# Kernel tuning notes

Measured on AMD Instinct MI355X. Metric: run time of the kernel, lower is better.

The kernel has to match this reference:

```python
import jax, jax.numpy as jnp
import numpy as np

N = 50000      # nodes
E = 800000     # message-passing edges
EF = 1000000   # decoder (full) edges
IN = 128       # in_channels
H = 64         # hidden_channels
OUT = 1        # out_channels
T = 128        # num_timesteps
RESCALE = 4000.0  # SinusoidalPosEmb rescale_steps


def sinusoidal_pos_emb(t, dim, num_steps):
    # t: [N] int -> [N, dim]
    x = t.astype(jnp.float32) * (RESCALE / num_steps)
    half = dim // 2
    freqs = jnp.exp(jnp.arange(half, dtype=jnp.float32) * (-jnp.log(10000.0) / (half - 1)))
    ang = x[:, None] * freqs[None, :]            # [N, half]
    return jnp.concatenate([jnp.sin(ang), jnp.cos(ang)], axis=-1)


def gcn_conv(h, W, b, row, col, norm, n):
    # standard GCNConv: linear -> gather src -> scale by sym norm -> scatter-add to dst -> +bias
    x = h @ W                                     # [N, H]
    msg = x[row] * norm[:, None]                  # [E+N, H]
    out = jax.ops.segment_sum(msg, col, num_segments=n)
    return out + b


def setup_inputs() -> dict:
    key = jax.random.key(0)
    ks = jax.random.split(key, 12)
    rn = lambda k, shape, s=0.02: jax.random.normal(k, shape, jnp.float32) * s
    return {
        "x": jax.random.normal(ks[0], (N, IN), jnp.float32),
        "edge_index": jax.random.randint(ks[1], (2, E), 0, N, jnp.int32),
        "full_edge_index": jax.random.randint(ks[2], (2, EF), 0, N, jnp.int32),
        "time_steps": jax.random.randint(ks[3], (N,), 0, T, jnp.int32),
        "W_in": rn(ks[4], (IN, H)), "b_in": jnp.zeros((H,), jnp.float32),
        "W_t1": rn(ks[5], (H, 4 * H)), "b_t1": jnp.zeros((4 * H,), jnp.float32),
        "W_t2": rn(ks[6], (4 * H, H)), "b_t2": jnp.zeros((H,), jnp.float32),
        "W_c0": rn(ks[7], (H, H)), "b_c0": jnp.zeros((H,), jnp.float32),
        "W_c1": rn(ks[8], (H, H)), "b_c1": jnp.zeros((H,), jnp.float32),
        "W_d1": rn(ks[9], (2 * H, H)), "b_d1": jnp.zeros((H,), jnp.float32),
        "W_d2": rn(ks[10], (H, OUT)), "b_d2": jnp.zeros((OUT,), jnp.float32),
    }


def reference(x, edge_index, full_edge_index, time_steps,
              W_in, b_in, W_t1, b_t1, W_t2, b_t2,
              W_c0, b_c0, W_c1, b_c1, W_d1, b_d1, W_d2, b_d2):
    n = x.shape[0]
    # --- embedder (dropout is identity in eval mode) ---
    h = x @ W_in + b_in                                        # [N, H]
    pe = sinusoidal_pos_emb(time_steps, H, T)                  # [N, H]
    t_emb = jax.nn.silu(pe @ W_t1 + b_t1) @ W_t2 + b_t2        # [N, H]
    h_embed = h + t_emb

    # --- GCN encoder: add self-loops once, symmetric normalization ---
    loops = jnp.arange(n, dtype=edge_index.dtype)
    row = jnp.concatenate([edge_index[0], loops])              # [E+N]
    col = jnp.concatenate([edge_index[1], loops])
    deg = jax.ops.segment_sum(jnp.ones_like(col, jnp.float32), col, num_segments=n)
    dinv = jnp.where(deg > 0, jax.lax.rsqrt(deg), 0.0)
    norm = dinv[row] * dinv[col]                               # [E+N]

    h = gcn_conv(h_embed, W_c0, b_c0, row, col, norm, n)
    h = jax.nn.relu(h)                                         # act between layers; norm=None -> identity
    h_enc = gcn_conv(h, W_c1, b_c1, row, col, norm, n)

    # --- edge decoder: gather src/dst, concat, 2-layer SiLU MLP ---
    src, dst = full_edge_index[0], full_edge_index[1]
    feat = jnp.concatenate([h_enc[src], h_enc[dst]], axis=-1)  # [EF, 2H]
    edge_logits = jax.nn.silu(feat @ W_d1 + b_d1) @ W_d2 + b_d2  # [EF, OUT]
    return edge_logits, h_embed, h_enc
```

## Files before the change

### kernel.cpp

```cpp
#include <hip/hip_runtime.h>
#include <hip/hip_bf16.h>
#include <math.h>

#define N_NODES 50000
#define E_MSG   800000
#define E_FULL  1000000
#define IN_C    128
#define H_C     64
#define T_STEPS 128

#define OFF_Win   0
#define OFF_bin   8192
#define OFF_Wt1   8256
#define OFF_bt1   24640
#define OFF_Wt2   24896
#define OFF_bt2   41280
#define OFF_Wc0   41344
#define OFF_bc0   45440
#define OFF_Wc1   45504
#define OFF_bc1   49600
#define OFF_Wd1   49664
#define OFF_bd1   57856
#define OFF_Wd2   57920
#define OFF_bd2   57984
#define W_TOTAL   57985
#define OFF_BSUM  58016
#define OFF_BCUR  58272
#define OFF_FWD1  58624
#define OFF_FWIN  60672
#define OFF_FWC0  64768
#define OFF_TEMB  66816
#define OFF_DINV  75008
#define OFF_FWC1  125008
#define OFF_PTR   175008
#define OFF_ELIST 225010
#define OFF_TMP2  1025012
#define OFF_ZBF   2625012
#define OFF_ZBF2  4225012
#define OFF_HENC8 5825012

#define SCAN_NB   ((N_NODES + 255) / 256)
#define BF_CH     ((E_MSG + SCAN_NB - 1) / SCAN_NB)
#define BC_NB     392
#define BC_CH     ((E_MSG + BC_NB - 1) / BC_NB)

typedef __attribute__((ext_vector_type(8))) short bf16x8;
typedef __attribute__((ext_vector_type(4))) float f32x4;

static __device__ __forceinline__ float bf2f(unsigned short u) {
    return __uint_as_float(((unsigned)u) << 16);
}
static __device__ __forceinline__ unsigned short f2bf(float f) {
    unsigned u = __float_as_uint(f);
    unsigned r = (u + 0x7fffu + ((u >> 16) & 1u)) >> 16;
    return (unsigned short)r;
}
static __device__ __forceinline__ unsigned char f2fp8(float f) {
    unsigned u = __float_as_uint(f);
    unsigned s = (u >> 24) & 0x80;
    float a = fminf(__uint_as_float(u & 0x7FFFFFFF), 448.0f);
    if (a < 0.015625f) {
        int qi = (int)rintf(a * 512.0f);
        return (unsigned char)(s | qi);
    }
    unsigned ua = __float_as_uint(a);
    int e = (int)((ua >> 23) & 0xFF) - 127;
    unsigned man = (ua & 0x7FFFFF) | 0x800000;
    unsigned r = man >> 20;
    unsigned rem = man & 0xFFFFF;
    if (rem > 0x80000u || (rem == 0x80000u && (r & 1))) r++;
    if (r == 16) { r = 8; e++; }
    if (e > 8) return (unsigned char)(s | 0x7E);
    return (unsigned char)(s | ((unsigned)(e + 7) << 3) | (r & 7));
}
static __device__ __forceinline__ bool detect_f32(const unsigned short* w, int* scnt) {
    if (threadIdx.x == 0) *scnt = 0;
    __syncthreads();
    int big = 0;
    for (int i = threadIdx.x; i < 2048; i += blockDim.x)
        if (fabsf(bf2f(w[2 * i])) > 0.5f) big++;
    atomicAdd(scnt, big);
    __syncthreads();
    return *scnt > 64;
}
static __device__ __forceinline__ float ldw(const void* p, int idx, bool f32) {
    return f32 ? ((const float*)p)[idx] : bf2f(((const unsigned short*)p)[idx]);
}

__global__ void __launch_bounds__(256) k_bfill(const int* __restrict__ row,
                                               const int* __restrict__ col,
                                               const int* __restrict__ btot,
                                               int* __restrict__ bcur,
                                               uint2* __restrict__ tmp) {
    __shared__ int pref[256];
    __shared__ int hist[SCAN_NB];
    __shared__ int basew[SCAN_NB];
    int b = blockIdx.x, t = threadIdx.x;

    int tv = (t < SCAN_NB) ? btot[t] : 0;
    pref[t] = tv;
    __syncthreads();
    for (int off = 1; off < 256; off <<= 1) {
        int u = (t >= off) ? pref[t - off] : 0;
        __syncthreads();
        pref[t] += u;
        __syncthreads();
    }
    int excl_t = pref[t] - tv;

    int lo = b * BF_CH;
    int hi = lo + BF_CH; if (hi > E_MSG) hi = E_MSG;
    for (int i = t; i < SCAN_NB; i += 256) hist[i] = 0;
    __syncthreads();
    for (int e = lo + t; e < hi; e += 256)
        atomicAdd(&hist[col[e] >> 8], 1);
    __syncthreads();
    if (t < SCAN_NB) {
        int c = hist[t];
        basew[t] = (c > 0) ? excl_t + atomicAdd(&bcur[t], c) : 0;
    }
    __syncthreads();
    for (int i = t; i < SCAN_NB; i += 256) hist[i] = 0;
    __syncthreads();
    for (int e = lo + t; e < hi; e += 256) {
        int src = row[e], c = col[e];
        int bk = c >> 8;
        int off = atomicAdd(&hist[bk], 1);
        tmp[basew[bk] + off] = uint2{(unsigned)src, (unsigned)c};
    }
}

__global__ void __launch_bounds__(256) k_csort2(const uint2* __restrict__ tmp,
                                                const int* __restrict__ btot,
                                                int* __restrict__ ptr,
                                                float* __restrict__ dinv,
                                                int* __restrict__ elist) {
    __shared__ int deg[256];
    __shared__ int pfx[256];
    int b = blockIdx.x, t = threadIdx.x;

    int tv = (t < SCAN_NB) ? btot[t] : 0;
    pfx[t] = tv;
    __syncthreads();
    for (int off = 1; off < 256; off <<= 1) {
        int u = (t >= off) ? pfx[t - off] : 0;
        __syncthreads();
        pfx[t] += u;
        __syncthreads();
    }
    __shared__ int se[2];
    if (t == b) { se[0] = pfx[t] - tv; se[1] = pfx[t]; }
    __syncthreads();
    int start = se[0], end = se[1];

    deg[t] = 0;
    __syncthreads();
    for (int e = start + t; e < end; e += 256)
        atomicAdd(&deg[tmp[e].y & 255], 1);
    __syncthreads();

    int v = deg[t];
    pfx[t] = v;
    __syncthreads();
    for (int off = 1; off < 256; off <<= 1) {
        int u = (t >= off) ? pfx[t - off] : 0;
        __syncthreads();
        pfx[t] += u;
        __syncthreads();
    }
    int excl = pfx[t] - v;
    int n = (b << 8) + t;
    if (n < N_NODES) {
        ptr[n] = start + excl;
        dinv[n] = rsqrtf((float)v + 1.0f);
    }
    if (b == 0 && t == 0) ptr[N_NODES] = E_MSG;
    __syncthreads();
    deg[t] = excl;
    __syncthreads();
    for (int e = start + t; e < end; e += 256) {
        uint2 p = tmp[e];
        int pos = atomicAdd(&deg[p.y & 255], 1);
        elist[start + pos] = (int)p.x;
    }
}

#define WP_BC_NB   392
#define WP_CVT_NB  227
#define WP_PREP_NB 96
#define WP_TEMB_NB 128
#define WP_TOTAL_NB (WP_BC_NB + WP_CVT_NB + WP_PREP_NB + WP_TEMB_NB)

struct CvtArgs { const void* src[14]; };

__global__ void __launch_bounds__(256) k_wprep(CvtArgs a,
                                               const int* __restrict__ ecol,
                                               int* __restrict__ bsum,
                                               float* ws) {
    __shared__ int scnt;
    int bid = blockIdx.x;
    int tid = threadIdx.x;

    if (bid < WP_BC_NB) {
        __shared__ int hist[SCAN_NB];
        for (int i = tid; i < SCAN_NB; i += 256) hist[i] = 0;
        __syncthreads();
        int lo = bid * BC_CH;
        int hi = lo + BC_CH; if (hi > E_MSG) hi = E_MSG;
        for (int e = lo + tid; e < hi; e += 256)
            atomicAdd(&hist[ecol[e] >> 8], 1);
        __syncthreads();
        for (int i = tid; i < SCAN_NB; i += 256) {
            int c = hist[i];
            if (c > 0) atomicAdd(&bsum[i], c);
        }
        return;
    }
    bid -= WP_BC_NB;

    bool f32 = detect_f32((const unsigned short*)a.src[0], &scnt);

    if (bid < WP_CVT_NB) {
        int t = bid * 256 + tid;
        if (t >= W_TOTAL) return;
        const int starts[14] = {OFF_Win, OFF_bin, OFF_Wt1, OFF_bt1, OFF_Wt2, OFF_bt2,
                                OFF_Wc0, OFF_bc0, OFF_Wc1, OFF_bc1, OFF_Wd1, OFF_bd1,
                                OFF_Wd2, OFF_bd2};
        int seg = 0;
#pragma unroll
        for (int i = 1; i < 14; i++)
            if (t >= starts[i]) seg = i;
        ws[t] = ldw(a.src[seg], t - starts[seg], f32);
    } else if (bid < WP_CVT_NB + WP_PREP_NB) {
        int idx = (bid - WP_CVT_NB) * 256 + tid;
        int local, j, lane, ct, c, t, m, q;
        if (idx < 8192) {
            local = idx;
            j = local & 7; lane = (local >> 3) & 63; ct = local >> 9;
            c = ct >> 2; t = ct & 3; m = lane & 15; q = lane >> 4;
            ((unsigned char*)(ws + OFF_FWD1))[local] =
                f2fp8(16.0f * ldw(a.src[10], (32 * c + 8 * q + j) * 64 + 16 * t + m, f32));
        } else if (idx < 16384) {
            local = idx - 8192;
            j = local & 7; lane = (local >> 3) & 63; ct = local >> 9;
            c = ct >> 2; t = ct & 3; m = lane & 15; q = lane >> 4;
            ((unsigned short*)(ws + OFF_FWIN))[local] =
                f2bf(ldw(a.src[0], (32 * c + 8 * q + j) * 64 + 16 * t + m, f32));
        } else if (idx < 20480) {
            local = idx - 16384;
            j = local & 7; lane = (local >> 3) & 63; ct = local >> 9;
            c = ct >> 2; t = ct & 3; m = lane & 15; q = lane >> 4;
            ((unsigned short*)(ws + OFF_FWC0))[local] =
                f2bf(ldw(a.src[6], (32 * c + 8 * q + j) * 64 + 16 * t + m, f32));
        } else {
            local = idx - 20480;
            j = local & 7; lane = (local >> 3) & 63; ct = local >> 9;
            c = ct >> 2; t = ct & 3; m = lane & 15; q = lane >> 4;
            ((unsigned short*)(ws + OFF_FWC1))[local] =
                f2bf(ldw(a.src[8], (32 * c + 8 * q + j) * 64 + 16 * t + m, f32));
        }
    } else {
        __shared__ float pe[64];
        __shared__ float us4[4][256];
        __shared__ float us[256];
        __shared__ float pcs[4][64];
        int j = tid & 63;
        int kg = tid >> 6;
        int t = bid - WP_CVT_NB - WP_PREP_NB;

        if (tid < 64) {
            float xt = (float)t * (4000.0f / 128.0f);
            float sc = -logf(10000.0f) / 31.0f;
            float fr = __expf((float)(tid & 31) * sc);
            float ang = xt * fr;
            pe[tid] = (tid < 32) ? sinf(ang) : cosf(ang);
        }
        __syncthreads();

        float pu[4] = {0.f, 0.f, 0.f, 0.f};
#pragma unroll
        for (int kk = 0; kk < 16; kk++) {
            int k = 16 * kg + kk;
            float p = pe[k];
#pragma unroll
            for (int q = 0; q < 4; q++)
                pu[q] = fmaf(p, ldw(a.src[2], k * 256 + q * 64 + j, f32), pu[q]);
        }
#pragma unroll
        for (int q = 0; q < 4; q++) us4[kg][q * 64 + j] = pu[q];
        __syncthreads();

        {
            float uu = ldw(a.src[3], tid, f32) +
                       us4[0][tid] + us4[1][tid] + us4[2][tid] + us4[3][tid];
            us[tid] = uu * __builtin_amdgcn_rcpf(1.0f + __expf(-uu));
        }
        __syncthreads();

        float pc = 0.f;
#pragma unroll
        for (int kk = 0; kk < 64; kk++) {
            int k = 64 * kg + kk;
            pc = fmaf(us[k], ldw(a.src[4], k * 64 + j, f32), pc);
        }
        pcs[kg][j] = pc;
        __syncthreads();
        if (tid < 64) {
            float acc = ldw(a.src[5], j, f32) +
                        pcs[0][j] + pcs[1][j] + pcs[2][j] + pcs[3][j];
            (ws + OFF_TEMB)[t * 64 + j] = acc;
        }
    }
}

__global__ void __launch_bounds__(256) k_embed(const void* __restrict__ xraw,
                                               const unsigned short* __restrict__ wdet,
                                               const int* __restrict__ tsteps,
                                               float* __restrict__ ws,
                                               float* __restrict__ out_hembed,
                                               unsigned short* __restrict__ zbf) {
    __shared__ int scnt;
    __shared__ unsigned short tl[4][16 * 64];
    bool f32 = detect_f32(wdet, &scnt);

    int lane = threadIdx.x & 63;
    int wv = threadIdx.x >> 6;
    int m = lane & 15, quad = lane >> 4;
    int wid = blockIdx.x * 4 + wv;
    if (wid > N_NODES / 16 - 1) wid = N_NODES / 16 - 1;
    int n0 = wid * 16;

    const unsigned short* fwin = (const unsigned short*)(ws + OFF_FWIN);
    const unsigned short* fwc0 = (const unsigned short*)(ws + OFF_FWC0);

    bf16x8 bI[4][4];
#pragma unroll
    for (int c = 0; c < 4; c++)
#pragma unroll
        for (int t = 0; t < 4; t++)
            bI[c][t] = *reinterpret_cast<const bf16x8*>(fwin + (c * 4 + t) * 512 + lane * 8);

    f32x4 acc[4] = {f32x4{0,0,0,0}, f32x4{0,0,0,0}, f32x4{0,0,0,0}, f32x4{0,0,0,0}};
#pragma unroll
    for (int c = 0; c < 4; c++) {
        bf16x8 a;
        if (f32) {
            const float* xp = (const float*)xraw + (size_t)(n0 + m) * 128 + 32 * c + 8 * quad;
            float4 v0 = *reinterpret_cast<const float4*>(xp);
            float4 v1 = *reinterpret_cast<const float4*>(xp + 4);
            a[0] = (short)f2bf(v0.x); a[1] = (short)f2bf(v0.y);
            a[2] = (short)f2bf(v0.z); a[3] = (short)f2bf(v0.w);
            a[4] = (short)f2bf(v1.x); a[5] = (short)f2bf(v1.y);
            a[6] = (short)f2bf(v1.z); a[7] = (short)f2bf(v1.w);
        } else {
            a = *reinterpret_cast<const bf16x8*>(
                (const unsigned short*)xraw + (size_t)(n0 + m) * 128 + 32 * c + 8 * quad);
        }
#pragma unroll
        for (int t = 0; t < 4; t++)
            acc[t] = __builtin_amdgcn_mfma_f32_16x16x32_bf16(a, bI[c][t], acc[t], 0, 0, 0);
    }

    int tn[4];
#pragma unroll
    for (int r = 0; r < 4; r++) tn[r] = tsteps[n0 + 4 * quad + r];
    const float* temb = ws + OFF_TEMB;
#pragma unroll
    for (int t = 0; t < 4; t++) {
        int ch = 16 * t + m;
        float bj = ws[OFF_bin + ch];
#pragma unroll
        for (int r = 0; r < 4; r++) {
            int node = n0 + 4 * quad + r;
            float v = acc[t][r] + bj + temb[tn[r] * 64 + ch];
            out_hembed[(size_t)node * 64 + ch] = v;
            tl[wv][(4 * quad + r) * 64 + ch] = f2bf(v);
        }
    }
    __syncthreads();

    bf16x8 bC[2][4];
#pragma unroll
    for (int c = 0; c < 2; c++)
#pragma unroll
        for (int t = 0; t < 4; t++)
            bC[c][t] = *reinterpret_cast<const bf16x8*>(fwc0 + (c * 4 + t) * 512 + lane * 8);

    f32x4 az[4] = {f32x4{0,0,0,0}, f32x4{0,0,0,0}, f32x4{0,0,0,0}, f32x4{0,0,0,0}};
#pragma unroll
    for (int c = 0; c < 2; c++) {
        bf16x8 a2 = *reinterpret_cast<const bf16x8*>(&tl[wv][m * 64 + 32 * c + 8 * quad]);
#pragma unroll
        for (int t = 0; t < 4; t++)
            az[t] = __builtin_amdgcn_mfma_f32_16x16x32_bf16(a2, bC[c][t], az[t], 0, 0, 0);
    }
    const float* dinv = ws + OFF_DINV;
    float dv[4];
#pragma unroll
    for (int r = 0; r < 4; r++) dv[r] = dinv[n0 + 4 * quad + r];
#pragma unroll
    for (int t = 0; t < 4; t++) {
        int ch = 16 * t + m;
#pragma unroll
        for (int r = 0; r < 4; r++)
            zbf[(size_t)(n0 + 4 * quad + r) * 64 + ch] = f2bf(az[t][r] * dv[r]);
    }
}

__global__ void __launch_bounds__(256) k_gather0(const unsigned short* __restrict__ zbf,
                                                 const int* __restrict__ ptr,
                                                 const int* __restrict__ elist,
                                                 const float* __restrict__ ws,
                                                 unsigned short* __restrict__ zout) {
    __shared__ unsigned short tile[16 * 64];
    const float* dinv = ws + OFF_DINV;
    const float* bias = ws + OFF_bc0;
    const unsigned short* fwc1 = (const unsigned short*)(ws + OFF_FWC1);

    int lane = threadIdx.x & 63;
    int wv = threadIdx.x >> 6;
    int g = lane >> 4;
    int cl = lane & 15;
    int n0 = blockIdx.x * 16;

    float4 b4 = *reinterpret_cast<const float4*>(bias + 4 * cl);

#pragma unroll
    for (int snode = 0; snode < 4; snode++) {
        int li = wv * 4 + snode;
        int n = n0 + li;
        int base = ptr[n], end = ptr[n + 1];

        float ws0 = (g == 0) ? 1.0f : 0.0f;
        ushort4 sv = *reinterpret_cast<const ushort4*>(zbf + (size_t)n * 64 + cl * 4);
        float s0 = ws0 * bf2f(sv.x), s1 = ws0 * bf2f(sv.y);
        float s2 = ws0 * bf2f(sv.z), s3 = ws0 * bf2f(sv.w);

        for (int k = base; k < end; k += 8) {
            int e0 = k + g, e1 = k + 4 + g;
            int r0 = elist[min(e0, end - 1)];
            int r1 = elist[min(e1, end - 1)];
            ushort4 v0 = *reinterpret_cast<const ushort4*>(zbf + (size_t)r0 * 64 + cl * 4);
            ushort4 v1 = *reinterpret_cast<const ushort4*>(zbf + (size_t)r1 * 64 + cl * 4);
            float w0 = (e0 < end) ? 1.0f : 0.0f;
            float w1 = (e1 < end) ? 1.0f : 0.0f;
            s0 = fmaf(w0, bf2f(v0.x), s0); s1 = fmaf(w0, bf2f(v0.y), s1);
            s2 = fmaf(w0, bf2f(v0.z), s2); s3 = fmaf(w0, bf2f(v0.w), s3);
            s0 = fmaf(w1, bf2f(v1.x), s0); s1 = fmaf(w1, bf2f(v1.y), s1);
            s2 = fmaf(w1, bf2f(v1.z), s2); s3 = fmaf(w1, bf2f(v1.w), s3);
        }
        s0 += __shfl_xor(s0, 16, 64); s0 += __shfl_xor(s0, 32, 64);
        s1 += __shfl_xor(s1, 16, 64); s1 += __shfl_xor(s1, 32, 64);
        s2 += __shfl_xor(s2, 16, 64); s2 += __shfl_xor(s2, 32, 64);
        s3 += __shfl_xor(s3, 16, 64); s3 += __shfl_xor(s3, 32, 64);

        if (g == 0) {
            float dv = dinv[n];
            float h0 = fmaxf(fmaf(dv, s0, b4.x), 0.0f);
            float h1 = fmaxf(fmaf(dv, s1, b4.y), 0.0f);
            float h2 = fmaxf(fmaf(dv, s2, b4.z), 0.0f);
            float h3 = fmaxf(fmaf(dv, s3, b4.w), 0.0f);
            ushort4 hv;
            hv.x = f2bf(h0); hv.y = f2bf(h1); hv.z = f2bf(h2); hv.w = f2bf(h3);
            int bo = li * 128 + ((cl * 8) ^ ((li & 7) << 4));
            *reinterpret_cast<ushort4*>((char*)tile + bo) = hv;
        }
    }
    __syncthreads();

    int m = lane & 15, q = lane >> 4;
    bf16x8 bB0 = *reinterpret_cast<const bf16x8*>(fwc1 + (0 * 4 + wv) * 512 + lane * 8);
    bf16x8 bB1 = *reinterpret_cast<const bf16x8*>(fwc1 + (1 * 4 + wv) * 512 + lane * 8);

    f32x4 az = f32x4{0, 0, 0, 0};
    {
        int bo0 = m * 128 + ((0 * 64 + q * 16) ^ ((m & 7) << 4));
        bf16x8 a0 = *reinterpret_cast<const bf16x8*>((const char*)tile + bo0);
        az = __builtin_amdgcn_mfma_f32_16x16x32_bf16(a0, bB0, az, 0, 0, 0);
        int bo1 = m * 128 + ((1 * 64 + q * 16) ^ ((m & 7) << 4));
        bf16x8 a1 = *reinterpret_cast<const bf16x8*>((const char*)tile + bo1);
        az = __builtin_amdgcn_mfma_f32_16x16x32_bf16(a1, bB1, az, 0, 0, 0);
    }
    float dv4[4];
#pragma unroll
    for (int r = 0; r < 4; r++) dv4[r] = dinv[n0 + 4 * q + r];
#pragma unroll
    for (int r = 0; r < 4; r++) {
        int node = n0 + 4 * q + r;
        zout[(size_t)node * 64 + 16 * wv + m] = f2bf(az[r] * dv4[r]);
    }
}

__global__ void __launch_bounds__(256) k_gather1(const unsigned short* __restrict__ zbf,
                                                 const int* __restrict__ ptr,
                                                 const int* __restrict__ elist,
                                                 const float* __restrict__ dinv,
                                                 const float* __restrict__ bias,
                                                 unsigned char* __restrict__ henc8,
                                                 float* __restrict__ ofp) {
    int lane = threadIdx.x & 63;
    int n = blockIdx.x * 4 + (threadIdx.x >> 6);
    int g = lane >> 4;
    int cl = lane & 15;
    int base = ptr[n], end = ptr[n + 1];

    float4 b4 = *reinterpret_cast<const float4*>(bias + 4 * cl);

    float ws0 = (g == 0) ? 1.0f : 0.0f;
    ushort4 sv = *reinterpret_cast<const ushort4*>(zbf + (size_t)n * 64 + cl * 4);
    float s0 = ws0 * bf2f(sv.x), s1 = ws0 * bf2f(sv.y);
    float s2 = ws0 * bf2f(sv.z), s3 = ws0 * bf2f(sv.w);

    for (int k = base; k < end; k += 8) {
        int e0 = k + g, e1 = k + 4 + g;
        int r0 = elist[min(e0, end - 1)];
        int r1 = elist[min(e1, end - 1)];
        ushort4 v0 = *reinterpret_cast<const ushort4*>(zbf + (size_t)r0 * 64 + cl * 4);
        ushort4 v1 = *reinterpret_cast<const ushort4*>(zbf + (size_t)r1 * 64 + cl * 4);
        float w0 = (e0 < end) ? 1.0f : 0.0f;
        float w1 = (e1 < end) ? 1.0f : 0.0f;
        s0 = fmaf(w0, bf2f(v0.x), s0); s1 = fmaf(w0, bf2f(v0.y), s1);
        s2 = fmaf(w0, bf2f(v0.z), s2); s3 = fmaf(w0, bf2f(v0.w), s3);
        s0 = fmaf(w1, bf2f(v1.x), s0); s1 = fmaf(w1, bf2f(v1.y), s1);
        s2 = fmaf(w1, bf2f(v1.z), s2); s3 = fmaf(w1, bf2f(v1.w), s3);
    }
    s0 += __shfl_xor(s0, 16, 64); s0 += __shfl_xor(s0, 32, 64);
    s1 += __shfl_xor(s1, 16, 64); s1 += __shfl_xor(s1, 32, 64);
    s2 += __shfl_xor(s2, 16, 64); s2 += __shfl_xor(s2, 32, 64);
    s3 += __shfl_xor(s3, 16, 64); s3 += __shfl_xor(s3, 32, 64);

    float dv = dinv[n];
    float o0 = fmaf(dv, s0, b4.x);
    float o1 = fmaf(dv, s1, b4.y);
    float o2 = fmaf(dv, s2, b4.z);
    float o3 = fmaf(dv, s3, b4.w);

    if (g == 0) {
        float4 ov; ov.x = o0; ov.y = o1; ov.z = o2; ov.w = o3;
        *reinterpret_cast<float4*>(ofp + (size_t)n * 64 + cl * 4) = ov;
    }
    int jc = lane >> 2;
    float a0 = __shfl(o0, jc, 64);
    float a1 = __shfl(o1, jc, 64);
    float a2 = __shfl(o2, jc, 64);
    float a3 = __shfl(o3, jc, 64);
    int sel = lane & 3;
    float mv = (sel == 0) ? a0 : (sel == 1) ? a1 : (sel == 2) ? a2 : a3;
    henc8[(size_t)n * 64 + lane] = f2fp8(16.0f * mv);
}

#define DEC_TPW 4
#define DEC_TILES (E_FULL / 16)

__global__ void __launch_bounds__(256) k_dec(const int* __restrict__ src,
                                             const int* __restrict__ dst,
                                             const unsigned char* __restrict__ h8,
                                             const float* __restrict__ ws,
                                             float* __restrict__ out) {
    __shared__ long s_bfr[16 * 64];
    __shared__ float s_w2[64];
    __shared__ float s_b1[64];

    int tid = threadIdx.x;
    float b2 = ws[OFF_bd2];
    {
        const long* fw8 = (const long*)(ws + OFF_FWD1);
        for (int idx = tid; idx < 1024; idx += 256)
            s_bfr[idx] = fw8[idx];
        if (tid < 64) {
            s_w2[tid] = ws[OFF_Wd2 + tid];
            s_b1[tid] = ws[OFF_bd1 + tid];
        }
    }
    __syncthreads();

    int lane = tid & 63;
    int wv = tid >> 6;
    int m = lane & 15;
    int quad = lane >> 4;

    int tile0 = (blockIdx.x * 4 + wv) * DEC_TPW;

    int sg[DEC_TPW], dg[DEC_TPW];
#pragma unroll
    for (int i = 0; i < DEC_TPW; i++) {
        int tc = min(tile0 + i, DEC_TILES - 1);
        sg[i] = src[tc * 16 + m];
        dg[i] = dst[tc * 16 + m];
    }

#pragma unroll
    for (int i = 0; i < DEC_TPW; i++) {
        int tile = tile0 + i;
        long A[4];
#pragma unroll
        for (int c = 0; c < 4; c++) {
            int row = (c < 2) ? sg[i] : dg[i];
            A[c] = *reinterpret_cast<const long*>(
                h8 + (size_t)row * 64 + (c & 1) * 32 + 8 * quad);
        }
        f32x4 acc[4] = {f32x4{0,0,0,0}, f32x4{0,0,0,0}, f32x4{0,0,0,0}, f32x4{0,0,0,0}};
#pragma unroll
        for (int c = 0; c < 4; c++)
#pragma unroll
            for (int mt = 0; mt < 4; mt++) {
                long bk = s_bfr[(c * 4 + mt) * 64 + lane];
                acc[mt] = __builtin_amdgcn_mfma_f32_16x16x32_fp8_fp8(bk, A[c], acc[mt], 0, 0, 0);
            }

        float p[4];
#pragma unroll
        for (int mt = 0; mt < 4; mt++) {
            float4 w2v = *reinterpret_cast<const float4*>(&s_w2[16 * mt + 4 * quad]);
            float4 b1v = *reinterpret_cast<const float4*>(&s_b1[16 * mt + 4 * quad]);
            float pm = 0.0f;
#pragma unroll
            for (int r = 0; r < 4; r++) {
                float v = fmaf(acc[mt][r], 0.00390625f, b1v[r]);
                float h = v * __builtin_amdgcn_rcpf(1.0f + __expf(-v));
                pm = fmaf(h, w2v[r], pm);
            }
            p[mt] = pm;
        }
        float sv = (p[0] + p[1]) + (p[2] + p[3]);
        sv += __shfl_xor(sv, 16, 64);
        sv += __shfl_xor(sv, 32, 64);
        if (lane < 16 && tile < DEC_TILES)
            out[tile * 16 + lane] = sv + b2;
    }
}

extern "C" void kernel_launch(void* const* d_in, const int* in_sizes, int n_in,
                              void* d_out, int out_size, void* d_ws, size_t ws_size,
                              hipStream_t stream) {
    if (n_in < 18) return;
    const void* x              = d_in[0];
    const int* edge_index      = (const int*)d_in[1];
    const int* full_edge_index = (const int*)d_in[2];
    const int* tsteps          = (const int*)d_in[3];
    float* ws = (float*)d_ws;
    float* out = (float*)d_out;

    int*   iws   = (int*)d_ws;
    int*   bsum  = iws + OFF_BSUM;
    int*   bcur  = iws + OFF_BCUR;
    int*   ptr   = iws + OFF_PTR;
    int*   elist = iws + OFF_ELIST;
    uint2* tmp   = (uint2*)(iws + OFF_TMP2);
    unsigned short* zbf  = (unsigned short*)(ws + OFF_ZBF);
    unsigned short* zbf2 = (unsigned short*)(ws + OFF_ZBF2);
    unsigned char*  h8   = (unsigned char*)(ws + OFF_HENC8);

    CvtArgs ca;
    for (int i = 0; i < 14; i++) ca.src[i] = d_in[4 + i];

    hipMemsetAsync(bsum, 0, (size_t)512 * 4, stream);

    k_wprep<<<WP_TOTAL_NB, 256, 0, stream>>>(ca, edge_index + E_MSG, bsum, ws);

    k_bfill<<<SCAN_NB, 256, 0, stream>>>(edge_index, edge_index + E_MSG, bsum,
                                         bcur, tmp);
    k_csort2<<<SCAN_NB, 256, 0, stream>>>(tmp, bsum, ptr, ws + OFF_DINV, elist);

    k_embed<<<(N_NODES / 16 + 3) / 4, 256, 0, stream>>>(
        x, (const unsigned short*)d_in[4], tsteps, ws, out + E_FULL, zbf);

    k_gather0<<<N_NODES / 16, 256, 0, stream>>>(zbf, ptr, elist, ws, zbf2);

    k_gather1<<<N_NODES / 4, 256, 0, stream>>>(
        zbf2, ptr, elist, ws + OFF_DINV, ws + OFF_bc1, h8,
        out + E_FULL + (size_t)N_NODES * 64);

    int dec_blocks = (DEC_TILES + 4 * DEC_TPW - 1) / (4 * DEC_TPW);
    k_dec<<<dec_blocks, 256, 0, stream>>>(full_edge_index, full_edge_index + E_FULL,
                                          h8, ws, out);
}
```

Before: 253.8 us.

## Software-pipeline decoder gathers and branch out masked neighbor loads in GCN gathers

The edge decoder now prefetches the next tile's fp8 node rows and the index pair two tiles ahead while running MFMA on the current tile, and each wave handles 8 tiles instead of 4. In both GCN gather kernels the masked weight-multiply for tail edges becomes a branch, so out-of-range lanes skip their loads and the self-term load runs only in group 0. The aim is to hide gather latency in the decoder and cut redundant memory traffic in the aggregation. The trade-offs are higher register pressure, fewer decoder blocks, and lane divergence in the tail iterations.

```diff
diff --git a/kernel.cpp b/kernel.cpp
--- a/kernel.cpp
+++ b/kernel.cpp
@@ -431,23 +431,28 @@
         int n = n0 + li;
         int base = ptr[n], end = ptr[n + 1];
 
-        float ws0 = (g == 0) ? 1.0f : 0.0f;
-        ushort4 sv = *reinterpret_cast<const ushort4*>(zbf + (size_t)n * 64 + cl * 4);
-        float s0 = ws0 * bf2f(sv.x), s1 = ws0 * bf2f(sv.y);
-        float s2 = ws0 * bf2f(sv.z), s3 = ws0 * bf2f(sv.w);
+        float s0 = 0.f, s1 = 0.f, s2 = 0.f, s3 = 0.f;
+        if (g == 0) {
+            ushort4 sv = *reinterpret_cast<const ushort4*>(zbf + (size_t)n * 64 + cl * 4);
+            s0 = bf2f(sv.x); s1 = bf2f(sv.y); s2 = bf2f(sv.z); s3 = bf2f(sv.w);
+        }
 
         for (int k = base; k < end; k += 8) {
             int e0 = k + g, e1 = k + 4 + g;
-            int r0 = elist[min(e0, end - 1)];
-            int r1 = elist[min(e1, end - 1)];
-            ushort4 v0 = *reinterpret_cast<const ushort4*>(zbf + (size_t)r0 * 64 + cl * 4);
-            ushort4 v1 = *reinterpret_cast<const ushort4*>(zbf + (size_t)r1 * 64 + cl * 4);
-            float w0 = (e0 < end) ? 1.0f : 0.0f;
-            float w1 = (e1 < end) ? 1.0f : 0.0f;
-            s0 = fmaf(w0, bf2f(v0.x), s0); s1 = fmaf(w0, bf2f(v0.y), s1);
-            s2 = fmaf(w0, bf2f(v0.z), s2); s3 = fmaf(w0, bf2f(v0.w), s3);
-            s0 = fmaf(w1, bf2f(v1.x), s0); s1 = fmaf(w1, bf2f(v1.y), s1);
-            s2 = fmaf(w1, bf2f(v1.z), s2); s3 = fmaf(w1, bf2f(v1.w), s3);
+            if (e1 < end) {
+                int r0 = elist[e0], r1 = elist[e1];
+                ushort4 v0 = *reinterpret_cast<const ushort4*>(zbf + (size_t)r0 * 64 + cl * 4);
+                ushort4 v1 = *reinterpret_cast<const ushort4*>(zbf + (size_t)r1 * 64 + cl * 4);
+                s0 += bf2f(v0.x) + bf2f(v1.x);
+                s1 += bf2f(v0.y) + bf2f(v1.y);
+                s2 += bf2f(v0.z) + bf2f(v1.z);
+                s3 += bf2f(v0.w) + bf2f(v1.w);
+            } else if (e0 < end) {
+                int r0 = elist[e0];
+                ushort4 v0 = *reinterpret_cast<const ushort4*>(zbf + (size_t)r0 * 64 + cl * 4);
+                s0 += bf2f(v0.x); s1 += bf2f(v0.y);
+                s2 += bf2f(v0.z); s3 += bf2f(v0.w);
+            }
         }
         s0 += __shfl_xor(s0, 16, 64); s0 += __shfl_xor(s0, 32, 64);
         s1 += __shfl_xor(s1, 16, 64); s1 += __shfl_xor(s1, 32, 64);
@@ -506,23 +511,28 @@
 
     float4 b4 = *reinterpret_cast<const float4*>(bias + 4 * cl);
 
-    float ws0 = (g == 0) ? 1.0f : 0.0f;
-    ushort4 sv = *reinterpret_cast<const ushort4*>(zbf + (size_t)n * 64 + cl * 4);
-    float s0 = ws0 * bf2f(sv.x), s1 = ws0 * bf2f(sv.y);
-    float s2 = ws0 * bf2f(sv.z), s3 = ws0 * bf2f(sv.w);
+    float s0 = 0.f, s1 = 0.f, s2 = 0.f, s3 = 0.f;
+    if (g == 0) {
+        ushort4 sv = *reinterpret_cast<const ushort4*>(zbf + (size_t)n * 64 + cl * 4);
+        s0 = bf2f(sv.x); s1 = bf2f(sv.y); s2 = bf2f(sv.z); s3 = bf2f(sv.w);
+    }
 
     for (int k = base; k < end; k += 8) {
         int e0 = k + g, e1 = k + 4 + g;
-        int r0 = elist[min(e0, end - 1)];
-        int r1 = elist[min(e1, end - 1)];
-        ushort4 v0 = *reinterpret_cast<const ushort4*>(zbf + (size_t)r0 * 64 + cl * 4);
-        ushort4 v1 = *reinterpret_cast<const ushort4*>(zbf + (size_t)r1 * 64 + cl * 4);
-        float w0 = (e0 < end) ? 1.0f : 0.0f;
-        float w1 = (e1 < end) ? 1.0f : 0.0f;
-        s0 = fmaf(w0, bf2f(v0.x), s0); s1 = fmaf(w0, bf2f(v0.y), s1);
-        s2 = fmaf(w0, bf2f(v0.z), s2); s3 = fmaf(w0, bf2f(v0.w), s3);
-        s0 = fmaf(w1, bf2f(v1.x), s0); s1 = fmaf(w1, bf2f(v1.y), s1);
-        s2 = fmaf(w1, bf2f(v1.z), s2); s3 = fmaf(w1, bf2f(v1.w), s3);
+        if (e1 < end) {
+            int r0 = elist[e0], r1 = elist[e1];
+            ushort4 v0 = *reinterpret_cast<const ushort4*>(zbf + (size_t)r0 * 64 + cl * 4);
+            ushort4 v1 = *reinterpret_cast<const ushort4*>(zbf + (size_t)r1 * 64 + cl * 4);
+            s0 += bf2f(v0.x) + bf2f(v1.x);
+            s1 += bf2f(v0.y) + bf2f(v1.y);
+            s2 += bf2f(v0.z) + bf2f(v1.z);
+            s3 += bf2f(v0.w) + bf2f(v1.w);
+        } else if (e0 < end) {
+            int r0 = elist[e0];
+            ushort4 v0 = *reinterpret_cast<const ushort4*>(zbf + (size_t)r0 * 64 + cl * 4);
+            s0 += bf2f(v0.x); s1 += bf2f(v0.y);
+            s2 += bf2f(v0.z); s3 += bf2f(v0.w);
+        }
     }
     s0 += __shfl_xor(s0, 16, 64); s0 += __shfl_xor(s0, 32, 64);
     s1 += __shfl_xor(s1, 16, 64); s1 += __shfl_xor(s1, 32, 64);
@@ -549,7 +559,7 @@
     henc8[(size_t)n * 64 + lane] = f2fp8(16.0f * mv);
 }
 
-#define DEC_TPW 4
+#define DEC_TPW 8
 #define DEC_TILES (E_FULL / 16)
 
 __global__ void __launch_bounds__(256) k_dec(const int* __restrict__ src,
@@ -581,31 +591,38 @@
 
     int tile0 = (blockIdx.x * 4 + wv) * DEC_TPW;
 
-    int sg[DEC_TPW], dg[DEC_TPW];
-#pragma unroll
-    for (int i = 0; i < DEC_TPW; i++) {
-        int tc = min(tile0 + i, DEC_TILES - 1);
-        sg[i] = src[tc * 16 + m];
-        dg[i] = dst[tc * 16 + m];
+    int tc = min(tile0, DEC_TILES - 1);
+    int s0i = src[tc * 16 + m], d0i = dst[tc * 16 + m];
+    tc = min(tile0 + 1, DEC_TILES - 1);
+    int s1i = src[tc * 16 + m], d1i = dst[tc * 16 + m];
+    long A0[4];
+#pragma unroll
+    for (int c = 0; c < 4; c++) {
+        int row = (c < 2) ? s0i : d0i;
+        A0[c] = *reinterpret_cast<const long*>(
+            h8 + (size_t)row * 64 + (c & 1) * 32 + 8 * quad);
     }
 
 #pragma unroll
     for (int i = 0; i < DEC_TPW; i++) {
         int tile = tile0 + i;
-        long A[4];
+        int t2 = min(tile0 + i + 2, DEC_TILES - 1);
+        int s2i = src[t2 * 16 + m], d2i = dst[t2 * 16 + m];
+        long A1[4];
 #pragma unroll
         for (int c = 0; c < 4; c++) {
-            int row = (c < 2) ? sg[i] : dg[i];
-            A[c] = *reinterpret_cast<const long*>(
+            int row = (c < 2) ? s1i : d1i;
+            A1[c] = *reinterpret_cast<const long*>(
                 h8 + (size_t)row * 64 + (c & 1) * 32 + 8 * quad);
         }
+
         f32x4 acc[4] = {f32x4{0,0,0,0}, f32x4{0,0,0,0}, f32x4{0,0,0,0}, f32x4{0,0,0,0}};
 #pragma unroll
         for (int c = 0; c < 4; c++)
 #pragma unroll
             for (int mt = 0; mt < 4; mt++) {
                 long bk = s_bfr[(c * 4 + mt) * 64 + lane];
-                acc[mt] = __builtin_amdgcn_mfma_f32_16x16x32_fp8_fp8(bk, A[c], acc[mt], 0, 0, 0);
+                acc[mt] = __builtin_amdgcn_mfma_f32_16x16x32_fp8_fp8(bk, A0[c], acc[mt], 0, 0, 0);
             }
 
         float p[4];
@@ -627,6 +644,10 @@
         sv += __shfl_xor(sv, 32, 64);
         if (lane < 16 && tile < DEC_TILES)
             out[tile * 16 + lane] = sv + b2;
+
+#pragma unroll
+        for (int c = 0; c < 4; c++) A0[c] = A1[c];
+        s1i = s2i; d1i = d2i;
     }
 }
 
```

Result: no change. 258.3 us (+1.8%).
